# Performance work log

Measured on AMD Instinct MI355X. Metric: run time of the kernel, lower is better.

The kernel has to match this reference:

```python
import jax, jax.numpy as jnp
import numpy as np

N, E, F, H, C, G = 50000, 800000, 128, 64, 10, 512
NEG_SLOPE = 0.2
BN_EPS = 1e-5


def setup_inputs() -> dict:
    key = jax.random.key(0)
    ks = jax.random.split(key, 20)
    s = 0.05
    inp = {
        "x": jax.random.normal(ks[0], (N, F), jnp.float32),
        "edge_index": jax.random.randint(ks[1], (2, E), 0, N),
        "batch": jnp.sort(jax.random.randint(ks[2], (N,), 0, G)),
        # GATv2 layer 1 (lin_l, lin_r, att, bias)
        "Wl1": jax.random.normal(ks[3], (H, F), jnp.float32) * s,
        "Wr1": jax.random.normal(ks[4], (H, F), jnp.float32) * s,
        "att1": jax.random.normal(ks[5], (H,), jnp.float32) * s,
        "b1": jnp.zeros((H,), jnp.float32),
        # GATv2 layer 2
        "Wl2": jax.random.normal(ks[6], (H, H), jnp.float32) * s,
        "Wr2": jax.random.normal(ks[7], (H, H), jnp.float32) * s,
        "att2": jax.random.normal(ks[8], (H,), jnp.float32) * s,
        "b2": jnp.zeros((H,), jnp.float32),
        # MLP head: Linear(H,H) -> BatchNorm1d(H) -> ReLU -> Linear(H,C)
        "W3": jax.random.normal(ks[9], (H, H), jnp.float32) * s,
        "b3": jnp.zeros((H,), jnp.float32),
        "gamma": jnp.ones((H,), jnp.float32),
        "beta": jnp.zeros((H,), jnp.float32),
        "W4": jax.random.normal(ks[10], (C, H), jnp.float32) * s,
        "b4": jnp.zeros((C,), jnp.float32),
    }
    return inp


def _gatv2_layer(x, src, dst, Wl, Wr, att, b, n_nodes):
    # GATv2: e_ij = att . LeakyReLU(Wl x_j + Wr x_i); softmax over j in N(i); out_i = sum alpha_ij * Wl x_j
    xl = x @ Wl.T  # [N, H] source transform
    xr = x @ Wr.T  # [N, H] dest transform
    e = jnp.einsum("eh,h->e", jax.nn.leaky_relu(xl[src] + xr[dst], NEG_SLOPE), att)  # [E]
    m = jax.ops.segment_max(e, dst, num_segments=n_nodes)
    m = jnp.where(jnp.isfinite(m), m, 0.0)
    a = jnp.exp(e - m[dst])
    denom = jax.ops.segment_sum(a, dst, num_segments=n_nodes)
    alpha = a / denom[dst]  # self-loops guarantee denom > 0
    out = jax.ops.segment_sum(alpha[:, None] * xl[src], dst, num_segments=n_nodes)
    return out + b


def reference(x, edge_index, batch, Wl1, Wr1, att1, b1, Wl2, Wr2, att2, b2,
              W3, b3, gamma, beta, W4, b4):
    n_nodes = x.shape[0]
    loop = jnp.arange(n_nodes, dtype=edge_index.dtype)
    src = jnp.concatenate([edge_index[0], loop])  # add_self_loops=True (PyG default)
    dst = jnp.concatenate([edge_index[1], loop])

    h = _gatv2_layer(x, src, dst, Wl1, Wr1, att1, b1, n_nodes)
    h = jax.nn.relu(h)
    h = _gatv2_layer(h, src, dst, Wl2, Wr2, att2, b2, n_nodes)

    # global_mean_pool over graphs
    sums = jax.ops.segment_sum(h, batch, num_segments=G)  # [G, H]
    counts = jax.ops.segment_sum(jnp.ones((n_nodes,), h.dtype), batch, num_segments=G)
    pooled = sums / jnp.maximum(counts, 1.0)[:, None]

    # MLP head: Linear -> BatchNorm1d (training: batch stats, biased var) -> ReLU -> Linear
    z = pooled @ W3.T + b3
    mu = jnp.mean(z, axis=0)
    var = jnp.mean((z - mu) ** 2, axis=0)
    z = (z - mu) / jnp.sqrt(var + BN_EPS) * gamma + beta
    z = jax.nn.relu(z)
    z = z @ W4.T + b4
    return jax.nn.log_softmax(z, axis=1)
```

## Files before the change

kernel.cpp:

```cpp
#include <hip/hip_runtime.h>
#include <hip/hip_bf16.h>

#define NODES 50000
#define EDGES 800000
#define FEAT 128
#define HID 64
#define NCLS 10
#define NGRAPH 512
#define ETOT (EDGES + NODES)
#define NEG_SLOPE 0.2f
#define BN_EPS 1e-5f
#define NT_TILES ((NODES + 63) / 64)
#define NBINS 98
#define BTILE 8192
#define BBLK ((ETOT + BTILE - 1) / BTILE)
#define BIN_CAP 14336
#define TBLK 512
#define EDGE_WAVES 8192

typedef __attribute__((ext_vector_type(8))) short short8;
typedef __attribute__((ext_vector_type(4))) float f32x4;

__device__ __forceinline__ short f2b(float v) {
  unsigned int u = __float_as_uint(v);
  return (short)((u + 0x7FFFu + ((u >> 16) & 1u)) >> 16);
}
__device__ __forceinline__ float b2f(short s) {
  return __uint_as_float(((unsigned int)(unsigned short)s) << 16);
}


__device__ __forceinline__ void transform_body(
    char* smem, int bid, const void* __restrict__ A, int a_bf16, int K,
    const float* __restrict__ Wl, const float* __restrict__ Wr,
    short* __restrict__ xl, short* __restrict__ xr) {
  short* s_a = (short*)smem;
  char* dyn2 = smem + 64 * (K + 8) * 2;
  short* s_w = (short*)dyn2;
  float* s_out = (float*)dyn2;
  const int pitch = K + 8;
  int tid = threadIdx.x;
  int w = tid >> 6, lane = tid & 63;
  int n16 = lane & 15, quad = lane >> 4;
  int half = w & 1, chunk = w >> 1;
  short* outp = half ? xr : xl;
  float* s_ow = s_out + w * 16 * 68;
  int ktn = K >> 5;
  int kq = K >> 2, ksh = (K == 128) ? 5 : 4;

  for (int i = tid; i < 128 * kq; i += 512) {
    int r = i / kq, c = i - r * kq;
    const float* src = (r < 64) ? Wl : Wr;
    float4 v = *((const float4*)(src + (r & 63) * K) + c);
    short4 bb;
    bb.x = f2b(v.x); bb.y = f2b(v.y); bb.z = f2b(v.z); bb.w = f2b(v.w);
    *(short4*)(s_w + r * pitch + c * 4) = bb;
  }
  __syncthreads();
  short8 bfrag[4][4];
  for (int t = 0; t < 4; ++t)
    for (int kt = 0; kt < ktn; ++kt)
      bfrag[t][kt] = *(const short8*)(s_w + (half * 64 + t * 16 + n16) * pitch + kt * 32 + quad * 8);

  for (int nt = bid; nt < NT_TILES; nt += TBLK) {
    int n0 = nt * 64;
    __syncthreads();
    if (a_bf16) {
      int ku = K >> 3;
      for (int i = tid; i < 64 * ku; i += 512) {
        int row = i / ku, c = i - row * ku;
        int grow = n0 + row;
        short8 v = (short8){0, 0, 0, 0, 0, 0, 0, 0};
        if (grow < NODES) v = ((const short8*)((const short*)A + (size_t)grow * K))[c];
        *(short8*)(s_a + row * pitch + c * 8) = v;
      }
    } else {
      for (int i = tid; i < (64 << ksh); i += 512) {
        int row = i >> ksh, kc = i & (kq - 1);
        int grow = n0 + row;
        float4 v = (grow < NODES) ? *((const float4*)((const float*)A + (size_t)grow * K) + kc)
                                  : make_float4(0.f, 0.f, 0.f, 0.f);
        short4 bb;
        bb.x = f2b(v.x); bb.y = f2b(v.y); bb.z = f2b(v.z); bb.w = f2b(v.w);
        *(short4*)(s_a + row * pitch + kc * 4) = bb;
      }
    }
    __syncthreads();
    f32x4 acc[4];
#pragma unroll
    for (int t = 0; t < 4; ++t) acc[t] = (f32x4){0.f, 0.f, 0.f, 0.f};
    const short* arow = s_a + (chunk * 16 + n16) * pitch + quad * 8;
    for (int kt = 0; kt < ktn; ++kt) {
      short8 af = *(const short8*)(arow + kt * 32);
#pragma unroll
      for (int t = 0; t < 4; ++t)
        acc[t] = __builtin_amdgcn_mfma_f32_16x16x32_bf16(af, bfrag[t][kt], acc[t], 0, 0, 0);
    }
#pragma unroll
    for (int t = 0; t < 4; ++t)
#pragma unroll
      for (int r = 0; r < 4; ++r)
        s_ow[(quad * 4 + r) * 68 + t * 16 + n16] = acc[t][r];
#pragma unroll
    for (int it = 0; it < 4; ++it) {
      int i = it * 64 + lane;
      int row = i >> 4, c4 = i & 15;
      int grow = n0 + chunk * 16 + row;
      if (grow < NODES) {
        float4 v = *(const float4*)(s_ow + row * 68 + c4 * 4);
        short4 bb;
        bb.x = f2b(v.x); bb.y = f2b(v.y); bb.z = f2b(v.z); bb.w = f2b(v.w);
        *(short4*)(outp + (size_t)grow * HID + c4 * 4) = bb;
      }
    }
  }
}


__device__ __forceinline__ void binscatter_body(
    char* smem, int bid, const int* __restrict__ ei,
    int* __restrict__ binCursor, unsigned int* __restrict__ binned) {
  int* h = (int*)smem;
  int* b0 = h + NBINS;
  int tid = threadIdx.x;
  for (int i = tid; i < NBINS; i += 512) h[i] = 0;
  __syncthreads();
  int base = bid * BTILE;
  for (int k = 0; k < BTILE; k += 512) {
    int i = base + k + tid;
    if (i < ETOT) {
      int d = (i < EDGES) ? ei[EDGES + i] : (i - EDGES);
      atomicAdd(&h[d >> 9], 1);
    }
  }
  __syncthreads();
  for (int i = tid; i < NBINS; i += 512) {
    b0[i] = h[i] ? atomicAdd(&binCursor[i], h[i]) : 0;
    h[i] = 0;
  }
  __syncthreads();
  for (int k = 0; k < BTILE; k += 512) {
    int i = base + k + tid;
    if (i < ETOT) {
      int s, d;
      if (i < EDGES) { s = ei[i]; d = ei[EDGES + i]; }
      else { s = d = i - EDGES; }
      int bin = d >> 9;
      int r = atomicAdd(&h[bin], 1);
      binned[(size_t)bin * BIN_CAP + b0[bin] + r] =
          (unsigned int)s | ((unsigned int)(d & 511) << 16);
    }
  }
}


__global__ void __launch_bounds__(512) k_front(
    const float* __restrict__ x, const float* __restrict__ Wl1,
    const float* __restrict__ Wr1, short* __restrict__ xl, short* __restrict__ xr,
    const int* __restrict__ ei, int* __restrict__ binCursor,
    unsigned int* __restrict__ binned) {
  extern __shared__ char smem[];
  if (blockIdx.x < TBLK)
    transform_body(smem, blockIdx.x, x, 0, FEAT, Wl1, Wr1, xl, xr);
  else
    binscatter_body(smem, blockIdx.x - TBLK, ei, binCursor, binned);
}

__global__ void __launch_bounds__(512) k_transform2(
    const short* __restrict__ h, const float* __restrict__ Wl2,
    const float* __restrict__ Wr2, short* __restrict__ xl, short* __restrict__ xr) {
  extern __shared__ char smem[];
  transform_body(smem, blockIdx.x, h, 1, HID, Wl2, Wr2, xl, xr);
}


__global__ void __launch_bounds__(512) k_csr(
    const int* __restrict__ binCursor, const unsigned int* __restrict__ binned,
    int* __restrict__ rowstart, unsigned short* __restrict__ rowcnt,
    unsigned short* __restrict__ srcs, const int* __restrict__ batch,
    int* __restrict__ gstart) {
  __shared__ int h[512], sc[512], cur[512];
  __shared__ unsigned short sl[BIN_CAP];
  int b = blockIdx.x, t = threadIdx.x;
  if (b == NBINS) {
    for (int g = t; g <= NGRAPH; g += 512) {
      int lo = 0, hi = NODES;
      while (lo < hi) { int mid = (lo + hi) >> 1; if (batch[mid] < g) lo = mid + 1; else hi = mid; }
      gstart[g] = lo;
    }
    return;
  }
  size_t e0 = (size_t)b * BIN_CAP;
  int cnt = binCursor[b];
  int n0 = b << 9;
  h[t] = 0;
  __syncthreads();
  for (int i = t; i < cnt; i += 512)
    atomicAdd(&h[binned[e0 + i] >> 16], 1);
  __syncthreads();
  sc[t] = h[t];
  __syncthreads();
  for (int off = 1; off < 512; off <<= 1) {
    int v = (t >= off) ? sc[t - off] : 0;
    __syncthreads();
    sc[t] += v;
    __syncthreads();
  }
  int excl = sc[t] - h[t];
  cur[t] = excl;
  int node = n0 + t;
  if (node < NODES) {
    rowstart[node] = (int)e0 + excl;
    rowcnt[node] = (unsigned short)h[t];
  }
  __syncthreads();
  for (int i = t; i < cnt; i += 512) {
    unsigned int p = binned[e0 + i];
    int slot = atomicAdd(&cur[p >> 16], 1);
    sl[slot] = (unsigned short)(p & 0xFFFFu);
  }
  __syncthreads();
  for (int i = t; i < cnt; i += 512)
    srcs[e0 + i] = sl[i];
}


__global__ void __launch_bounds__(256) k_edge(
    const int* __restrict__ rowstart, const unsigned short* __restrict__ rowcnt,
    const unsigned short* __restrict__ srcs,
    const short* __restrict__ xlb, const short* __restrict__ xrb,
    const float* __restrict__ att, const float* __restrict__ bias,
    short* __restrict__ outb, int do_relu) {
  int wv = blockIdx.x * 4 + (threadIdx.x >> 6);
  int lane = threadIdx.x & 63;
  int fg = lane & 7;
  int eslot = lane >> 3;
  float at8[8], bb8[8];
  {
    float4 a0 = *(const float4*)(att + fg * 8);
    float4 a1 = *(const float4*)(att + fg * 8 + 4);
    at8[0] = a0.x; at8[1] = a0.y; at8[2] = a0.z; at8[3] = a0.w;
    at8[4] = a1.x; at8[5] = a1.y; at8[6] = a1.z; at8[7] = a1.w;
    float4 b0 = *(const float4*)(bias + fg * 8);
    float4 b1 = *(const float4*)(bias + fg * 8 + 4);
    bb8[0] = b0.x; bb8[1] = b0.y; bb8[2] = b0.z; bb8[3] = b0.w;
    bb8[4] = b1.x; bb8[5] = b1.y; bb8[6] = b1.z; bb8[7] = b1.w;
  }
  int wid = wv;
  if (wid >= NODES) return;
  int nbeg = rowstart[wid];
  int ncnt = rowcnt[wid];
  short8 nxr = *(const short8*)(xrb + (size_t)wid * HID + fg * 8);
  while (true) {
    int beg = nbeg, end = nbeg + ncnt;
    short8 xrs = nxr;
    int nwid = wid + EDGE_WAVES;
    if (nwid < NODES) {
      nbeg = rowstart[nwid];
      ncnt = rowcnt[nwid];
      nxr = *(const short8*)(xrb + (size_t)nwid * HID + fg * 8);
    }
    float xr8[8], acc8[8];
#pragma unroll
    for (int q = 0; q < 8; ++q) { xr8[q] = b2f(xrs[q]); acc8[q] = 0.f; }
    float denom = 0.f;
    for (int base = beg; base < end; base += 64) {
      int cnt = end - base; if (cnt > 64) cnt = 64;
      int myidx = (lane < cnt) ? (int)srcs[base + lane] : 0;
      int j0 = eslot;
      int sP = __shfl(myidx, (j0 < cnt) ? j0 : 0, 64);
      short8 xs = *(const short8*)(xlb + (size_t)sP * HID + fg * 8);
      for (int j = 0; j < cnt; j += 8) {
        bool valid = (j + eslot) < cnt;
        short8 cur = xs;
        if (j + 8 < cnt) {
          int jn = j + 8 + eslot;
          int sn = __shfl(myidx, (jn < cnt) ? jn : 0, 64);
          xs = *(const short8*)(xlb + (size_t)sn * HID + fg * 8);
        }
        float c8[8];
        float part = 0.f;
#pragma unroll
        for (int q = 0; q < 8; ++q) {
          c8[q] = b2f(cur[q]);
          float v = c8[q] + xr8[q];
          v = (v > 0.f) ? v : NEG_SLOPE * v;
          part += v * at8[q];
        }
        part += __shfl_xor(part, 1, 64);
        part += __shfl_xor(part, 2, 64);
        part += __shfl_xor(part, 4, 64);
        float p = valid ? __expf(part) : 0.f;
        denom += p;
#pragma unroll
        for (int q = 0; q < 8; ++q) acc8[q] += p * c8[q];
      }
    }
    denom += __shfl_xor(denom, 8, 64);
    denom += __shfl_xor(denom, 16, 64);
    denom += __shfl_xor(denom, 32, 64);
#pragma unroll
    for (int q = 0; q < 8; ++q) {
      acc8[q] += __shfl_xor(acc8[q], 8, 64);
      acc8[q] += __shfl_xor(acc8[q], 16, 64);
      acc8[q] += __shfl_xor(acc8[q], 32, 64);
    }
    if (eslot == 0) {
      float inv = 1.f / denom;
      short8 o;
#pragma unroll
      for (int q = 0; q < 8; ++q) {
        float ov = acc8[q] * inv + bb8[q];
        if (do_relu) ov = fmaxf(ov, 0.f);
        o[q] = f2b(ov);
      }
      *(short8*)(outb + (size_t)wid * HID + fg * 8) = o;
    }
    if (nwid >= NODES) break;
    wid = nwid;
  }
}


__global__ void k_pool(const short* __restrict__ h, const int* __restrict__ gstart,
                       float* __restrict__ pool) {
  int g = blockIdx.x * (blockDim.x >> 6) + (threadIdx.x >> 6);
  if (g >= NGRAPH) return;
  int lane = threadIdx.x & 63;
  int fg = lane & 7, ns = lane >> 3;
  int beg = gstart[g], end = gstart[g + 1];
  float acc[8] = {0.f, 0.f, 0.f, 0.f, 0.f, 0.f, 0.f, 0.f};
  for (int n = beg + ns; n < end; n += 8) {
    short8 v = *(const short8*)(h + (size_t)n * HID + fg * 8);
#pragma unroll
    for (int q = 0; q < 8; ++q) acc[q] += b2f(v[q]);
  }
#pragma unroll
  for (int q = 0; q < 8; ++q) {
    acc[q] += __shfl_xor(acc[q], 8, 64);
    acc[q] += __shfl_xor(acc[q], 16, 64);
    acc[q] += __shfl_xor(acc[q], 32, 64);
  }
  if (ns == 0) {
    float inv = 1.f / fmaxf((float)(end - beg), 1.f);
    float4 o0 = {acc[0] * inv, acc[1] * inv, acc[2] * inv, acc[3] * inv};
    float4 o1 = {acc[4] * inv, acc[5] * inv, acc[6] * inv, acc[7] * inv};
    *(float4*)(pool + g * HID + fg * 8) = o0;
    *(float4*)(pool + g * HID + fg * 8 + 4) = o1;
  }
}


__global__ void k_head1(const float* __restrict__ pool,
                        const float* __restrict__ W3, const float* __restrict__ b3,
                        float* __restrict__ z) {
  __shared__ float s_w3[HID * (HID + 1)];
  for (int idx = threadIdx.x; idx < HID * HID; idx += blockDim.x) {
    int f = idx >> 6, k = idx & 63;
    s_w3[f * (HID + 1) + k] = W3[idx];
  }
  __syncthreads();
  int i = blockIdx.x * blockDim.x + threadIdx.x;
  if (i >= NGRAPH * HID) return;
  int g = i >> 6, f = i & 63;
  float acc = b3[f];
  for (int k = 0; k < HID; ++k)
    acc += pool[g * HID + k] * s_w3[f * (HID + 1) + k];
  z[i] = acc;
}

__global__ void k_head2(const float* __restrict__ z, const float* __restrict__ gamma,
                        const float* __restrict__ beta, float* __restrict__ ss) {
  int f = threadIdx.x;
  if (f >= HID) return;
  float s = 0.f, s2 = 0.f;
  for (int g = 0; g < NGRAPH; ++g) {
    float v = z[g * HID + f];
    s += v; s2 += v * v;
  }
  float mu = s / NGRAPH;
  float var = s2 / NGRAPH - mu * mu;
  float rstd = rsqrtf(var + BN_EPS);
  float sc = gamma[f] * rstd;
  ss[f] = sc;
  ss[HID + f] = beta[f] - mu * sc;
}

__global__ void k_head3(const float* __restrict__ z, const float* __restrict__ ss,
                        const float* __restrict__ W4, const float* __restrict__ b4,
                        float* __restrict__ out) {
  int g = blockIdx.x * blockDim.x + threadIdx.x;
  if (g >= NGRAPH) return;
  float acc[NCLS];
#pragma unroll
  for (int c = 0; c < NCLS; ++c) acc[c] = b4[c];
  for (int f = 0; f < HID; ++f) {
    float zn = fmaxf(z[g * HID + f] * ss[f] + ss[HID + f], 0.f);
#pragma unroll
    for (int c = 0; c < NCLS; ++c) acc[c] += zn * W4[c * HID + f];
  }
  float m = acc[0];
#pragma unroll
  for (int c = 1; c < NCLS; ++c) m = fmaxf(m, acc[c]);
  float sum = 0.f;
#pragma unroll
  for (int c = 0; c < NCLS; ++c) sum += __expf(acc[c] - m);
  float lse = m + __logf(sum);
#pragma unroll
  for (int c = 0; c < NCLS; ++c) out[g * NCLS + c] = acc[c] - lse;
}

extern "C" void kernel_launch(void* const* d_in, const int* in_sizes, int n_in,
                              void* d_out, int out_size, void* d_ws, size_t ws_size,
                              hipStream_t stream) {
  (void)in_sizes; (void)n_in; (void)out_size; (void)ws_size;
  const float* x     = (const float*)d_in[0];
  const int*   ei    = (const int*)d_in[1];
  const int*   batch = (const int*)d_in[2];
  const float* Wl1   = (const float*)d_in[3];
  const float* Wr1   = (const float*)d_in[4];
  const float* att1  = (const float*)d_in[5];
  const float* b1    = (const float*)d_in[6];
  const float* Wl2   = (const float*)d_in[7];
  const float* Wr2   = (const float*)d_in[8];
  const float* att2  = (const float*)d_in[9];
  const float* b2    = (const float*)d_in[10];
  const float* W3    = (const float*)d_in[11];
  const float* b3    = (const float*)d_in[12];
  const float* gamma = (const float*)d_in[13];
  const float* beta  = (const float*)d_in[14];
  const float* W4    = (const float*)d_in[15];
  const float* b4    = (const float*)d_in[16];
  float* out = (float*)d_out;

  char* ws = (char*)d_ws;
  size_t off = 0;
  auto alloc = [&](size_t bytes) -> char* {
    char* p = ws + off;
    off += (bytes + 255) & ~(size_t)255;
    return p;
  };
  int*      binCursor = (int*)alloc((size_t)NBINS * 4);
  unsigned int*   binned = (unsigned int*)alloc((size_t)NBINS * BIN_CAP * 4);
  unsigned short* srcs   = (unsigned short*)alloc((size_t)NBINS * BIN_CAP * 2);
  int*      rowstart  = (int*)alloc((size_t)NODES * 4);
  unsigned short* rowcnt = (unsigned short*)alloc((size_t)NODES * 2);
  int*      gstart    = (int*)alloc((size_t)(NGRAPH + 1) * 4);
  short*    bufA      = (short*)alloc((size_t)NODES * HID * 2);
  short*    bufB      = (short*)alloc((size_t)NODES * HID * 2);
  short*    bufC      = (short*)alloc((size_t)NODES * HID * 2);
  float*    pool      = (float*)alloc((size_t)NGRAPH * HID * 4);
  float*    z         = (float*)alloc((size_t)NGRAPH * HID * 4);
  float*    ss        = (float*)alloc((size_t)2 * HID * 4);

  int lds1 = 64 * (FEAT + 8) * 2 + 34816;
  int lds2 = 64 * (HID + 8) * 2 + 34816;

  hipMemsetAsync(binCursor, 0, (size_t)NBINS * 4, stream);
  k_front<<<TBLK + BBLK, 512, lds1, stream>>>(x, Wl1, Wr1, bufA, bufB, ei, binCursor, binned);
  k_csr<<<NBINS + 1, 512, 0, stream>>>(binCursor, binned, rowstart, rowcnt, srcs, batch, gstart);
  k_edge<<<EDGE_WAVES / 4, 256, 0, stream>>>(rowstart, rowcnt, srcs, bufA, bufB, att1, b1, bufC, 1);
  k_transform2<<<TBLK, 512, lds2, stream>>>(bufC, Wl2, Wr2, bufA, bufB);
  k_edge<<<EDGE_WAVES / 4, 256, 0, stream>>>(rowstart, rowcnt, srcs, bufA, bufB, att2, b2, bufC, 0);
  k_pool<<<NGRAPH / 4, 256, 0, stream>>>(bufC, gstart, pool);
  k_head1<<<(NGRAPH * HID + 255) / 256, 256, 0, stream>>>(pool, W3, b3, z);
  k_head2<<<1, 64, 0, stream>>>(z, gamma, beta, ss);
  k_head3<<<(NGRAPH + 255) / 256, 256, 0, stream>>>(z, ss, W4, b4, out);
}
```

Before: 260.4 us.

## Fuse pooling with first head linear, merge BN and classifier, pack edge math

The edge kernel's per-lane arithmetic now runs on two-wide float vectors, so the compiler can emit packed FP32 ops, and leaky ReLU becomes max(v, 0.2v). The head is collapsed from four kernels into two. Pooling also computes the W3 linear layer through shared memory, and one 512-thread block computes the BatchNorm stats, ReLU, W4 projection and log-softmax. This removes two launches and the intermediate pool and scale buffers. In exchange, the tail now runs serially in a single block.

```diff
diff --git a/kernel.cpp b/kernel.cpp
--- a/kernel.cpp
+++ b/kernel.cpp
@@ -20,6 +20,8 @@
 
 typedef __attribute__((ext_vector_type(8))) short short8;
 typedef __attribute__((ext_vector_type(4))) float f32x4;
+typedef __attribute__((ext_vector_type(2))) float f32x2;
+typedef __attribute__((ext_vector_type(4))) unsigned int u32x4;
 
 __device__ __forceinline__ short f2b(float v) {
   unsigned int u = __float_as_uint(v);
@@ -235,16 +237,16 @@
   int lane = threadIdx.x & 63;
   int fg = lane & 7;
   int eslot = lane >> 3;
-  float at8[8], bb8[8];
+  f32x2 at2[4], bb2[4];
   {
     float4 a0 = *(const float4*)(att + fg * 8);
     float4 a1 = *(const float4*)(att + fg * 8 + 4);
-    at8[0] = a0.x; at8[1] = a0.y; at8[2] = a0.z; at8[3] = a0.w;
-    at8[4] = a1.x; at8[5] = a1.y; at8[6] = a1.z; at8[7] = a1.w;
+    at2[0] = (f32x2){a0.x, a0.y}; at2[1] = (f32x2){a0.z, a0.w};
+    at2[2] = (f32x2){a1.x, a1.y}; at2[3] = (f32x2){a1.z, a1.w};
     float4 b0 = *(const float4*)(bias + fg * 8);
     float4 b1 = *(const float4*)(bias + fg * 8 + 4);
-    bb8[0] = b0.x; bb8[1] = b0.y; bb8[2] = b0.z; bb8[3] = b0.w;
-    bb8[4] = b1.x; bb8[5] = b1.y; bb8[6] = b1.z; bb8[7] = b1.w;
+    bb2[0] = (f32x2){b0.x, b0.y}; bb2[1] = (f32x2){b0.z, b0.w};
+    bb2[2] = (f32x2){b1.x, b1.y}; bb2[3] = (f32x2){b1.z, b1.w};
   }
   int wid = wv;
   if (wid >= NODES) return;
@@ -260,9 +262,14 @@
       ncnt = rowcnt[nwid];
       nxr = *(const short8*)(xrb + (size_t)nwid * HID + fg * 8);
     }
-    float xr8[8], acc8[8];
-#pragma unroll
-    for (int q = 0; q < 8; ++q) { xr8[q] = b2f(xrs[q]); acc8[q] = 0.f; }
+    f32x2 xr2[4], acc2[4];
+    u32x4 ur = *(u32x4*)&xrs;
+#pragma unroll
+    for (int q = 0; q < 4; ++q) {
+      xr2[q] = (f32x2){__uint_as_float(ur[q] << 16),
+                       __uint_as_float(ur[q] & 0xFFFF0000u)};
+      acc2[q] = (f32x2){0.f, 0.f};
+    }
     float denom = 0.f;
     for (int base = beg; base < end; base += 64) {
       int cnt = end - base; if (cnt > 64) cnt = 64;
@@ -278,41 +285,50 @@
           int sn = __shfl(myidx, (jn < cnt) ? jn : 0, 64);
           xs = *(const short8*)(xlb + (size_t)sn * HID + fg * 8);
         }
-        float c8[8];
-        float part = 0.f;
-#pragma unroll
-        for (int q = 0; q < 8; ++q) {
-          c8[q] = b2f(cur[q]);
-          float v = c8[q] + xr8[q];
-          v = (v > 0.f) ? v : NEG_SLOPE * v;
-          part += v * at8[q];
+        u32x4 uc = *(u32x4*)&cur;
+        f32x2 c2[4];
+        f32x2 dp = {0.f, 0.f};
+#pragma unroll
+        for (int q = 0; q < 4; ++q) {
+          c2[q] = (f32x2){__uint_as_float(uc[q] << 16),
+                          __uint_as_float(uc[q] & 0xFFFF0000u)};
+          f32x2 v = c2[q] + xr2[q];
+          v = __builtin_elementwise_max(v, v * NEG_SLOPE);
+          dp += v * at2[q];
         }
+        float part = dp[0] + dp[1];
         part += __shfl_xor(part, 1, 64);
         part += __shfl_xor(part, 2, 64);
         part += __shfl_xor(part, 4, 64);
         float p = valid ? __expf(part) : 0.f;
         denom += p;
-#pragma unroll
-        for (int q = 0; q < 8; ++q) acc8[q] += p * c8[q];
+        f32x2 pv = {p, p};
+#pragma unroll
+        for (int q = 0; q < 4; ++q) acc2[q] += pv * c2[q];
       }
     }
     denom += __shfl_xor(denom, 8, 64);
     denom += __shfl_xor(denom, 16, 64);
     denom += __shfl_xor(denom, 32, 64);
 #pragma unroll
-    for (int q = 0; q < 8; ++q) {
-      acc8[q] += __shfl_xor(acc8[q], 8, 64);
-      acc8[q] += __shfl_xor(acc8[q], 16, 64);
-      acc8[q] += __shfl_xor(acc8[q], 32, 64);
+    for (int q = 0; q < 4; ++q) {
+      acc2[q][0] += __shfl_xor(acc2[q][0], 8, 64);
+      acc2[q][0] += __shfl_xor(acc2[q][0], 16, 64);
+      acc2[q][0] += __shfl_xor(acc2[q][0], 32, 64);
+      acc2[q][1] += __shfl_xor(acc2[q][1], 8, 64);
+      acc2[q][1] += __shfl_xor(acc2[q][1], 16, 64);
+      acc2[q][1] += __shfl_xor(acc2[q][1], 32, 64);
     }
     if (eslot == 0) {
       float inv = 1.f / denom;
       short8 o;
 #pragma unroll
-      for (int q = 0; q < 8; ++q) {
-        float ov = acc8[q] * inv + bb8[q];
-        if (do_relu) ov = fmaxf(ov, 0.f);
-        o[q] = f2b(ov);
+      for (int q = 0; q < 4; ++q) {
+        float o0 = acc2[q][0] * inv + bb2[q][0];
+        float o1 = acc2[q][1] * inv + bb2[q][1];
+        if (do_relu) { o0 = fmaxf(o0, 0.f); o1 = fmaxf(o1, 0.f); }
+        o[2 * q] = f2b(o0);
+        o[2 * q + 1] = f2b(o1);
       }
       *(short8*)(outb + (size_t)wid * HID + fg * 8) = o;
     }
@@ -322,10 +338,13 @@
 }
 
 
-__global__ void k_pool(const short* __restrict__ h, const int* __restrict__ gstart,
-                       float* __restrict__ pool) {
-  int g = blockIdx.x * (blockDim.x >> 6) + (threadIdx.x >> 6);
-  if (g >= NGRAPH) return;
+__global__ void __launch_bounds__(256) k_pool(
+    const short* __restrict__ h, const int* __restrict__ gstart,
+    const float* __restrict__ W3, const float* __restrict__ b3,
+    float* __restrict__ z) {
+  __shared__ float s_pool[4 * 64];
+  int w = threadIdx.x >> 6;
+  int g = blockIdx.x * 4 + w;
   int lane = threadIdx.x & 63;
   int fg = lane & 7, ns = lane >> 3;
   int beg = gstart[g], end = gstart[g + 1];
@@ -343,61 +362,67 @@
   }
   if (ns == 0) {
     float inv = 1.f / fmaxf((float)(end - beg), 1.f);
-    float4 o0 = {acc[0] * inv, acc[1] * inv, acc[2] * inv, acc[3] * inv};
-    float4 o1 = {acc[4] * inv, acc[5] * inv, acc[6] * inv, acc[7] * inv};
-    *(float4*)(pool + g * HID + fg * 8) = o0;
-    *(float4*)(pool + g * HID + fg * 8 + 4) = o1;
-  }
-}
-
-
-__global__ void k_head1(const float* __restrict__ pool,
-                        const float* __restrict__ W3, const float* __restrict__ b3,
-                        float* __restrict__ z) {
-  __shared__ float s_w3[HID * (HID + 1)];
-  for (int idx = threadIdx.x; idx < HID * HID; idx += blockDim.x) {
-    int f = idx >> 6, k = idx & 63;
-    s_w3[f * (HID + 1) + k] = W3[idx];
-  }
-  __syncthreads();
-  int i = blockIdx.x * blockDim.x + threadIdx.x;
-  if (i >= NGRAPH * HID) return;
-  int g = i >> 6, f = i & 63;
-  float acc = b3[f];
-  for (int k = 0; k < HID; ++k)
-    acc += pool[g * HID + k] * s_w3[f * (HID + 1) + k];
-  z[i] = acc;
-}
-
-__global__ void k_head2(const float* __restrict__ z, const float* __restrict__ gamma,
-                        const float* __restrict__ beta, float* __restrict__ ss) {
-  int f = threadIdx.x;
-  if (f >= HID) return;
+#pragma unroll
+    for (int q = 0; q < 8; ++q) s_pool[w * 64 + fg * 8 + q] = acc[q] * inv;
+  }
+  __syncthreads();
+  float zacc = b3[lane];
+  const float* w3r = W3 + lane * HID;
+  const float* pg = s_pool + w * 64;
+#pragma unroll 4
+  for (int k = 0; k < HID; k += 4) {
+    float4 wv = *(const float4*)(w3r + k);
+    zacc += pg[k] * wv.x + pg[k + 1] * wv.y + pg[k + 2] * wv.z + pg[k + 3] * wv.w;
+  }
+  z[g * HID + lane] = zacc;
+}
+
+
+__global__ void __launch_bounds__(512) k_tail(
+    const float* __restrict__ z, const float* __restrict__ gamma,
+    const float* __restrict__ beta, const float* __restrict__ W4,
+    const float* __restrict__ b4, float* __restrict__ out) {
+  __shared__ float s_p1[8][64];
+  __shared__ float s_p2[8][64];
+  __shared__ float s_sc[64], s_sh[64];
+  __shared__ float s_w4[NCLS * HID];
+  int t = threadIdx.x;
+  int f = t & 63, seg = t >> 6;
   float s = 0.f, s2 = 0.f;
-  for (int g = 0; g < NGRAPH; ++g) {
+  for (int g = seg * 64; g < seg * 64 + 64; ++g) {
     float v = z[g * HID + f];
     s += v; s2 += v * v;
   }
-  float mu = s / NGRAPH;
-  float var = s2 / NGRAPH - mu * mu;
-  float rstd = rsqrtf(var + BN_EPS);
-  float sc = gamma[f] * rstd;
-  ss[f] = sc;
-  ss[HID + f] = beta[f] - mu * sc;
-}
-
-__global__ void k_head3(const float* __restrict__ z, const float* __restrict__ ss,
-                        const float* __restrict__ W4, const float* __restrict__ b4,
-                        float* __restrict__ out) {
-  int g = blockIdx.x * blockDim.x + threadIdx.x;
-  if (g >= NGRAPH) return;
+  s_p1[seg][f] = s;
+  s_p2[seg][f] = s2;
+  for (int i = t; i < NCLS * HID; i += 512) s_w4[i] = W4[i];
+  __syncthreads();
+  if (t < 64) {
+    float ss = 0.f, ss2 = 0.f;
+#pragma unroll
+    for (int k = 0; k < 8; ++k) { ss += s_p1[k][t]; ss2 += s_p2[k][t]; }
+    float mu = ss / NGRAPH;
+    float var = ss2 / NGRAPH - mu * mu;
+    float rstd = rsqrtf(var + BN_EPS);
+    float sc = gamma[t] * rstd;
+    s_sc[t] = sc;
+    s_sh[t] = beta[t] - mu * sc;
+  }
+  __syncthreads();
   float acc[NCLS];
 #pragma unroll
   for (int c = 0; c < NCLS; ++c) acc[c] = b4[c];
-  for (int f = 0; f < HID; ++f) {
-    float zn = fmaxf(z[g * HID + f] * ss[f] + ss[HID + f], 0.f);
-#pragma unroll
-    for (int c = 0; c < NCLS; ++c) acc[c] += zn * W4[c * HID + f];
+  const float* zr = z + t * HID;
+  for (int f0 = 0; f0 < HID; f0 += 4) {
+    float4 zv = *(const float4*)(zr + f0);
+    float zn0 = fmaxf(zv.x * s_sc[f0] + s_sh[f0], 0.f);
+    float zn1 = fmaxf(zv.y * s_sc[f0 + 1] + s_sh[f0 + 1], 0.f);
+    float zn2 = fmaxf(zv.z * s_sc[f0 + 2] + s_sh[f0 + 2], 0.f);
+    float zn3 = fmaxf(zv.w * s_sc[f0 + 3] + s_sh[f0 + 3], 0.f);
+#pragma unroll
+    for (int c = 0; c < NCLS; ++c)
+      acc[c] += zn0 * s_w4[c * HID + f0] + zn1 * s_w4[c * HID + f0 + 1] +
+                zn2 * s_w4[c * HID + f0 + 2] + zn3 * s_w4[c * HID + f0 + 3];
   }
   float m = acc[0];
 #pragma unroll
@@ -407,7 +432,7 @@
   for (int c = 0; c < NCLS; ++c) sum += __expf(acc[c] - m);
   float lse = m + __logf(sum);
 #pragma unroll
-  for (int c = 0; c < NCLS; ++c) out[g * NCLS + c] = acc[c] - lse;
+  for (int c = 0; c < NCLS; ++c) out[t * NCLS + c] = acc[c] - lse;
 }
 
 extern "C" void kernel_launch(void* const* d_in, const int* in_sizes, int n_in,
@@ -449,9 +474,7 @@
   short*    bufA      = (short*)alloc((size_t)NODES * HID * 2);
   short*    bufB      = (short*)alloc((size_t)NODES * HID * 2);
   short*    bufC      = (short*)alloc((size_t)NODES * HID * 2);
-  float*    pool      = (float*)alloc((size_t)NGRAPH * HID * 4);
   float*    z         = (float*)alloc((size_t)NGRAPH * HID * 4);
-  float*    ss        = (float*)alloc((size_t)2 * HID * 4);
 
   int lds1 = 64 * (FEAT + 8) * 2 + 34816;
   int lds2 = 64 * (HID + 8) * 2 + 34816;
@@ -462,8 +485,6 @@
   k_edge<<<EDGE_WAVES / 4, 256, 0, stream>>>(rowstart, rowcnt, srcs, bufA, bufB, att1, b1, bufC, 1);
   k_transform2<<<TBLK, 512, lds2, stream>>>(bufC, Wl2, Wr2, bufA, bufB);
   k_edge<<<EDGE_WAVES / 4, 256, 0, stream>>>(rowstart, rowcnt, srcs, bufA, bufB, att2, b2, bufC, 0);
-  k_pool<<<NGRAPH / 4, 256, 0, stream>>>(bufC, gstart, pool);
-  k_head1<<<(NGRAPH * HID + 255) / 256, 256, 0, stream>>>(pool, W3, b3, z);
-  k_head2<<<1, 64, 0, stream>>>(z, gamma, beta, ss);
-  k_head3<<<(NGRAPH + 255) / 256, 256, 0, stream>>>(z, ss, W4, b4, out);
-}
+  k_pool<<<NGRAPH / 4, 256, 0, stream>>>(bufC, gstart, W3, b3, z);
+  k_tail<<<1, 512, 0, stream>>>(z, gamma, beta, W4, b4, out);
+}
```

Measured after the change: 249.8 us. 4.1% less time.
